# Kernel tuning notes

Hardware: AMD Instinct MI355X
Metric: run time of the kernel (lower is better)

Reference implementation:

```python
import jax, jax.numpy as jnp
import numpy as np

N_NODES = 50000
N_EDGES = 800000
QRY = 128
KEY = 128
VAL = 128
HEADS = 8
HEAD_FEATS = VAL // HEADS
BN_EPS = 1e-5


def setup_inputs() -> dict:
    key = jax.random.key(0)
    ks = jax.random.split(key, 12)
    inp = {
        "ft_q": jax.random.normal(ks[0], (N_NODES, QRY), dtype=jnp.float32),
        "ft_k": jax.random.normal(ks[1], (N_NODES, KEY), dtype=jnp.float32),
        "src": jax.random.randint(ks[2], (N_EDGES,), 0, N_NODES, dtype=jnp.int32),
        "dst": jax.random.randint(ks[3], (N_EDGES,), 0, N_NODES, dtype=jnp.int32),
        # learned params
        "Wq": jax.random.normal(ks[4], (VAL, QRY), dtype=jnp.float32) / np.sqrt(QRY),
        "bq": jnp.zeros((VAL,), dtype=jnp.float32),
        "Wk": jax.random.normal(ks[5], (VAL, KEY), dtype=jnp.float32) / np.sqrt(KEY),
        "Wv": jax.random.normal(ks[6], (VAL, QRY), dtype=jnp.float32) / np.sqrt(QRY),
        "attn_e": jax.random.normal(ks[7], (VAL,), dtype=jnp.float32),
        "bn_q_g": jnp.ones((QRY,), dtype=jnp.float32),
        "bn_q_b": jnp.zeros((QRY,), dtype=jnp.float32),
        "bn_k_g": jnp.ones((KEY,), dtype=jnp.float32),
        "bn_k_b": jnp.zeros((KEY,), dtype=jnp.float32),
    }
    return inp


def _batch_norm(x, gamma, beta):
    # training-mode BatchNorm1d: normalize over batch dim
    mean = jnp.mean(x, axis=0, keepdims=True)
    var = jnp.var(x, axis=0, keepdims=True)
    return (x - mean) * jax.lax.rsqrt(var + BN_EPS) * gamma + beta


def reference(ft_q, ft_k, src, dst, Wq, bq, Wk, Wv, attn_e,
              bn_q_g, bn_q_b, bn_k_g, bn_k_b):
    ft_q = _batch_norm(ft_q, bn_q_g, bn_q_b)
    ft_k = _batch_norm(ft_k, bn_k_g, bn_k_b)

    q = ft_q @ Wq.T + bq                      # [N, VAL]
    k = ft_k @ Wk.T                           # [N, VAL]
    v = (ft_q @ Wv.T).reshape(-1, HEADS, HEAD_FEATS)  # [N, H, D]

    # u_add_v: per-edge e = q[src] + k[dst]
    e = q[src] + k[dst]                       # [E, VAL]
    e = (attn_e * jax.nn.sigmoid(e)).reshape(-1, HEADS, HEAD_FEATS).sum(-1)  # [E, H]

    # edge_softmax grouped by destination node
    m = jax.ops.segment_max(e, dst, num_segments=N_NODES)   # [N, H]
    ex = jnp.exp(e - m[dst])                                # [E, H]
    s = jax.ops.segment_sum(ex, dst, num_segments=N_NODES)  # [N, H]
    a = ex / s[dst]                                         # [E, H]

    # u_mul_e_sum: scatter-sum of v[src] * a over destination
    msg = v[src] * a[:, :, None]                            # [E, H, D]
    rst = jax.ops.segment_sum(msg, dst, num_segments=N_NODES)  # [N, H, D]
    return rst.reshape(-1, VAL)
```

## Files before the change

### kernel.cpp

```cpp
#include <hip/hip_runtime.h>

#define N_NODES 50000
#define N_EDGES 800000
#define FEATS 128
#define NCHUNK 196
#define CPAD 50176
#define GEMM_BX 196
#define GEMM_BLOCKS 588
#define SCAT_BLOCKS 3125
#define NTILE 782
#define NF_WAVES 8192

typedef __attribute__((ext_vector_type(8))) short bf16x8;
typedef __attribute__((ext_vector_type(4))) float f32x4;

__device__ __forceinline__ unsigned short f2bf(float f){
  unsigned u = __float_as_uint(f);
  u += 0x7FFF + ((u >> 16) & 1);
  return (unsigned short)(u >> 16);
}
__device__ __forceinline__ void unpack8(uint4 p, float* f){
  f[0]=__uint_as_float(p.x << 16); f[1]=__uint_as_float(p.x & 0xffff0000u);
  f[2]=__uint_as_float(p.y << 16); f[3]=__uint_as_float(p.y & 0xffff0000u);
  f[4]=__uint_as_float(p.z << 16); f[5]=__uint_as_float(p.z & 0xffff0000u);
  f[6]=__uint_as_float(p.w << 16); f[7]=__uint_as_float(p.w & 0xffff0000u);
}

__global__ __launch_bounds__(256) void stats_hist_kernel(
    const float* __restrict__ ftq, const float* __restrict__ ftk,
    float* __restrict__ sums, const int* __restrict__ dstE,
    int* __restrict__ counts, int* __restrict__ csums){
  __shared__ float red[4*FEATS];
  __shared__ int lchunk[NCHUNK];
  int tid = threadIdx.x, bid = blockIdx.x;
  if (bid < 768){
    for (int i = tid; i < 4*FEATS; i += 256) red[i] = 0.f;
    __syncthreads();
    int c = tid & 127, half = tid >> 7;
    float sq=0.f, qq=0.f, sk=0.f, kk2=0.f;
    for (int r = bid*2 + half; r < N_NODES; r += 1536){
      float xq = ftq[(size_t)r*FEATS + c];
      float xk = ftk[(size_t)r*FEATS + c];
      sq += xq; qq += xq*xq; sk += xk; kk2 += xk*xk;
    }
    atomicAdd(&red[0*FEATS+c], sq);
    atomicAdd(&red[1*FEATS+c], qq);
    atomicAdd(&red[2*FEATS+c], sk);
    atomicAdd(&red[3*FEATS+c], kk2);
    __syncthreads();
    if (tid < FEATS){
      atomicAdd(&sums[0*FEATS+tid], red[0*FEATS+tid]);
      atomicAdd(&sums[1*FEATS+tid], red[1*FEATS+tid]);
      atomicAdd(&sums[2*FEATS+tid], red[2*FEATS+tid]);
      atomicAdd(&sums[3*FEATS+tid], red[3*FEATS+tid]);
    }
  } else {
    for (int i = tid; i < NCHUNK; i += 256) lchunk[i] = 0;
    __syncthreads();
    for (int t = (bid-768)*256 + tid; t < N_EDGES; t += 256*256){
      int d = dstE[t];
      atomicAdd(&counts[d], 1);
      atomicAdd(&lchunk[d >> 8], 1);
    }
    __syncthreads();
    for (int i = tid; i < NCHUNK; i += 256)
      if (lchunk[i]) atomicAdd(&csums[i], lchunk[i]);
  }
}

__global__ __launch_bounds__(256) void scan_fold_kernel(
    const int* __restrict__ counts, const int* __restrict__ csums,
    int* __restrict__ loc, int* __restrict__ bscan,
    const float* __restrict__ Wq, const float* __restrict__ bq,
    const float* __restrict__ Wk, const float* __restrict__ Wv,
    const float* __restrict__ gq, const float* __restrict__ bqn,
    const float* __restrict__ gk, const float* __restrict__ bkn,
    const float* __restrict__ sums,
    unsigned short* __restrict__ Wb, float* __restrict__ bias){
  __shared__ int s[256];
  int tid = threadIdx.x, bid = blockIdx.x;
  if (bid < NCHUNK){
    int i = bid*256 + tid;
    int v = counts[i];
    s[tid] = v; __syncthreads();
    for (int d = 1; d < 256; d <<= 1){
      int tv = (tid >= d) ? s[tid-d] : 0; __syncthreads();
      s[tid] += tv; __syncthreads();
    }
    loc[i] = s[tid] - v;
  } else if (bid == NCHUNK){
    int v = (tid < NCHUNK) ? csums[tid] : 0;
    s[tid] = v; __syncthreads();
    for (int d = 1; d < 256; d <<= 1){
      int tv = (tid >= d) ? s[tid-d] : 0; __syncthreads();
      s[tid] += tv; __syncthreads();
    }
    if (tid < NCHUNK) bscan[tid] = s[tid] - v;
  } else {
    int wv = (bid - NCHUNK - 1)*4 + (tid >> 6);
    int lane = tid & 63;
    int m = wv >> 7;
    int o = wv & 127;
    const float* Wsrc = (m==0) ? Wq : (m==1) ? Wv : Wk;
    const float* g   = (m==2) ? gk : gq;
    const float* bb  = (m==2) ? bkn : bqn;
    const float* s0  = (m==2) ? (sums + 2*FEATS) : sums;
    const float invN = 1.0f / (float)N_NODES;
    float acc = 0.f;
    unsigned short w2[2];
    int i0 = lane*2;
    #pragma unroll
    for (int t = 0; t < 2; t++){
      int i = i0 + t;
      float mean = s0[i]*invN;
      float var  = s0[FEATS+i]*invN - mean*mean;
      float rstd = rsqrtf(var + 1e-5f);
      float scale = g[i]*rstd;
      float shift = bb[i] - mean*scale;
      float w = Wsrc[o*FEATS + i];
      w2[t] = f2bf(w*scale);
      acc += shift*w;
    }
    ((unsigned*)Wb)[(m*FEATS*FEATS + o*FEATS + i0) >> 1] =
        (unsigned)w2[0] | ((unsigned)w2[1] << 16);
    #pragma unroll
    for (int off = 1; off < 64; off <<= 1) acc += __shfl_xor(acc, off);
    if (lane == 0) bias[m*FEATS + o] = acc + ((m==0) ? bq[o] : 0.f);
  }
}

__global__ __launch_bounds__(256) void gemm_scatter_kernel(
    const float* __restrict__ ftq, const float* __restrict__ ftk,
    const unsigned short* __restrict__ Wball, const float* __restrict__ biasall,
    unsigned short* __restrict__ qv, unsigned short* __restrict__ kb,
    const int* __restrict__ dstE, const int* __restrict__ srcE,
    const int* __restrict__ loc, const int* __restrict__ bscan,
    int* __restrict__ cursor, int* __restrict__ src_csr){
  __shared__ unsigned short Bs[FEATS][136];
  int tid = threadIdx.x, bid = blockIdx.x;
  if (bid >= GEMM_BLOCKS){
    int t = (bid - GEMM_BLOCKS)*256 + tid;
    int d = dstE[t];
    int p = atomicAdd(&cursor[d], 1);
    src_csr[loc[d] + bscan[d >> 8] + p] = srcE[t];
    return;
  }
  int m = bid / GEMM_BX;
  int bx = bid - m*GEMM_BX;
  const float* X = (m==2) ? ftk : ftq;
  {
    const uint4* srcp = (const uint4*)(Wball + m*FEATS*FEATS);
    for (int idx = tid; idx < FEATS*FEATS/8; idx += 256){
      int n = idx >> 4;
      int kk = (idx & 15) * 8;
      *(uint4*)&Bs[n][kk] = srcp[idx];
    }
  }
  __syncthreads();
  int wave = tid >> 6, lane = tid & 63;
  int mrow = lane & 15, quad = lane >> 4;
  unsigned short* Out = (m==2) ? kb : (qv + m*128);
  const int ostride = (m==2) ? FEATS : 256;
  float bv[8];
  #pragma unroll
  for (int ct = 0; ct < 8; ct++) bv[ct] = biasall[m*FEATS + ct*16 + mrow];
  for (int t = bx; t < NTILE; t += GEMM_BX){
    int row0 = t*64;
    int arow = row0 + wave*16 + mrow;
    bool rok = arow < N_NODES;
    size_t abase = (size_t)(rok ? arow : 0) * FEATS;
    bf16x8 afrag[4];
    #pragma unroll
    for (int kt = 0; kt < 4; kt++){
      const float* xp = X + abase + kt*32 + quad*8;
      float4 x0 = *(const float4*)xp;
      float4 x1 = *(const float4*)(xp + 4);
      if (!rok){ x0 = make_float4(0.f,0.f,0.f,0.f); x1 = x0; }
      bf16x8 a;
      a[0]=(short)f2bf(x0.x); a[1]=(short)f2bf(x0.y); a[2]=(short)f2bf(x0.z); a[3]=(short)f2bf(x0.w);
      a[4]=(short)f2bf(x1.x); a[5]=(short)f2bf(x1.y); a[6]=(short)f2bf(x1.z); a[7]=(short)f2bf(x1.w);
      afrag[kt] = a;
    }
    f32x4 acc[8];
    #pragma unroll
    for (int i = 0; i < 8; i++) acc[i] = (f32x4){0.f,0.f,0.f,0.f};
    #pragma unroll
    for (int kt = 0; kt < 4; kt++){
      int kbk = kt*32 + quad*8;
      #pragma unroll
      for (int ct = 0; ct < 8; ct++){
        bf16x8 b = *(bf16x8*)&Bs[ct*16 + mrow][kbk];
        acc[ct] = __builtin_amdgcn_mfma_f32_16x16x32_bf16(afrag[kt], b, acc[ct], 0, 0, 0);
      }
    }
    #pragma unroll
    for (int ct = 0; ct < 8; ct++){
      int col = ct*16 + mrow;
      #pragma unroll
      for (int v = 0; v < 4; v++){
        int orow = row0 + wave*16 + quad*4 + v;
        unsigned ub = f2bf(acc[ct][v] + bv[ct]);
        unsigned partner = (unsigned)__shfl_xor((int)ub, 1);
        if (!(mrow & 1) && orow < N_NODES)
          *(unsigned*)&Out[(size_t)orow*ostride + col] = ub | (partner << 16);
      }
    }
  }
}

__global__ __launch_bounds__(256) void node_fused_kernel(
    const unsigned short* __restrict__ qv, const unsigned short* __restrict__ kb,
    const float* __restrict__ attn, const int* __restrict__ src_csr,
    const int* __restrict__ loc, const int* __restrict__ bscan,
    float* __restrict__ out){
  int tid = threadIdx.x;
  int lane = tid & 63;
  int h = lane & 7, g = lane >> 3;
  int w = blockIdx.x*4 + (tid >> 6);
  const float L2E = 1.44269504f;
  float ar[16];
  {
    const uint4* ap = (const uint4*)(attn + h*16);
    uint4 a0 = ap[0], a1 = ap[1], a2 = ap[2], a3 = ap[3];
    ar[0]=__uint_as_float(a0.x); ar[1]=__uint_as_float(a0.y); ar[2]=__uint_as_float(a0.z); ar[3]=__uint_as_float(a0.w);
    ar[4]=__uint_as_float(a1.x); ar[5]=__uint_as_float(a1.y); ar[6]=__uint_as_float(a1.z); ar[7]=__uint_as_float(a1.w);
    ar[8]=__uint_as_float(a2.x); ar[9]=__uint_as_float(a2.y); ar[10]=__uint_as_float(a2.z); ar[11]=__uint_as_float(a2.w);
    ar[12]=__uint_as_float(a3.x); ar[13]=__uint_as_float(a3.y); ar[14]=__uint_as_float(a3.z); ar[15]=__uint_as_float(a3.w);
  }
  for (int n = w; n < N_NODES; n += NF_WAVES){
    int off0 = loc[n]   + bscan[n>>8];
    int off1 = loc[n+1] + bscan[(n+1)>>8];
    int deg = off1 - off0;
    if (deg == 0){
      ((float2*)(out + (size_t)n*FEATS))[lane] = make_float2(0.f, 0.f);
      continue;
    }
    float kf2[16];
    {
      const unsigned short* kr = kb + (size_t)n*FEATS + h*16;
      uint4 k0 = *(const uint4*)kr;
      uint4 k1 = *(const uint4*)(kr + 8);
      float kf[16]; unpack8(k0, kf); unpack8(k1, kf+8);
      #pragma unroll
      for (int i = 0; i < 16; i++) kf2[i] = -L2E * kf[i];
    }
    float ssum = 0.f;
    float acc[16];
    #pragma unroll
    for (int i = 0; i < 16; i++) acc[i] = 0.f;
    int s_next = (g < deg) ? src_csr[off0 + g] : 0;
    for (int j = g; j < deg; j += 8){
      int s = s_next;
      if (j + 8 < deg) s_next = src_csr[off0 + j + 8];
      const unsigned short* qr = qv + (size_t)s*256 + h*16;
      uint4 q0 = *(const uint4*)qr;
      uint4 q1 = *(const uint4*)(qr + 8);
      uint4 v0 = *(const uint4*)(qr + 128);
      uint4 v1 = *(const uint4*)(qr + 136);
      float qf[16]; unpack8(q0, qf); unpack8(q1, qf+8);
      float t = 0.f;
      #pragma unroll
      for (int i = 0; i < 16; i++){
        float xs = fmaf(qf[i], -L2E, kf2[i]);
        float sg = __builtin_amdgcn_rcpf(1.f + __builtin_amdgcn_exp2f(xs));
        t = fmaf(ar[i], sg, t);
      }
      float ex = __builtin_amdgcn_exp2f(t * L2E);
      ssum += ex;
      float vf[16]; unpack8(v0, vf); unpack8(v1, vf+8);
      #pragma unroll
      for (int i = 0; i < 16; i++) acc[i] = fmaf(ex, vf[i], acc[i]);
    }
    ssum += __shfl_xor(ssum, 8); ssum += __shfl_xor(ssum, 16); ssum += __shfl_xor(ssum, 32);
    #pragma unroll
    for (int i = 0; i < 16; i++){
      acc[i] += __shfl_xor(acc[i], 8);
      acc[i] += __shfl_xor(acc[i], 16);
      acc[i] += __shfl_xor(acc[i], 32);
    }
    if (g == 0){
      float inv_s = 1.f / ssum;
      float4* op = (float4*)(out + (size_t)n*FEATS + h*16);
      op[0] = make_float4(acc[0]*inv_s, acc[1]*inv_s, acc[2]*inv_s, acc[3]*inv_s);
      op[1] = make_float4(acc[4]*inv_s, acc[5]*inv_s, acc[6]*inv_s, acc[7]*inv_s);
      op[2] = make_float4(acc[8]*inv_s, acc[9]*inv_s, acc[10]*inv_s, acc[11]*inv_s);
      op[3] = make_float4(acc[12]*inv_s, acc[13]*inv_s, acc[14]*inv_s, acc[15]*inv_s);
    }
  }
}

extern "C" void kernel_launch(void* const* d_in, const int* in_sizes, int n_in,
                              void* d_out, int out_size, void* d_ws, size_t ws_size,
                              hipStream_t stream){
  (void)in_sizes; (void)n_in; (void)out_size; (void)ws_size;
  const float* ftq  = (const float*)d_in[0];
  const float* ftk  = (const float*)d_in[1];
  const int*   srcE = (const int*)d_in[2];
  const int*   dstE = (const int*)d_in[3];
  const float* Wq   = (const float*)d_in[4];
  const float* bq   = (const float*)d_in[5];
  const float* Wk   = (const float*)d_in[6];
  const float* Wv   = (const float*)d_in[7];
  const float* attn = (const float*)d_in[8];
  const float* gq   = (const float*)d_in[9];
  const float* bqn  = (const float*)d_in[10];
  const float* gk   = (const float*)d_in[11];
  const float* bkn  = (const float*)d_in[12];

  char* ws = (char*)d_ws;
  int*   counts  = (int*)(ws + 0);
  int*   cursor  = (int*)(ws + 200704);
  float* sums    = (float*)(ws + 400704);
  int*   csums   = (int*)(ws + 402752);
  int*   loc     = (int*)(ws + 403536);
  int*   bscan   = (int*)(ws + 604240);
  int*   src_csr = (int*)(ws + 605024);
  unsigned short* Wb = (unsigned short*)(ws + 3805024);
  float* biasf   = (float*)(ws + 3903328);
  unsigned short* qv = (unsigned short*)(ws + 3904864);
  unsigned short* kb = qv + (size_t)N_NODES*256;
  float* out = (float*)d_out;

  hipMemsetAsync(ws, 0, 403536, stream);

  hipLaunchKernelGGL(stats_hist_kernel, dim3(1024), dim3(256), 0, stream,
                     ftq, ftk, sums, dstE, counts, csums);
  hipLaunchKernelGGL(scan_fold_kernel, dim3(293), dim3(256), 0, stream,
                     counts, csums, loc, bscan,
                     Wq, bq, Wk, Wv, gq, bqn, gk, bkn, sums, Wb, biasf);
  hipLaunchKernelGGL(gemm_scatter_kernel, dim3(GEMM_BLOCKS + SCAT_BLOCKS), dim3(256), 0, stream,
                     ftq, ftk, Wb, biasf, qv, kb, dstE, srcE, loc, bscan, cursor, src_csr);
  hipLaunchKernelGGL(node_fused_kernel, dim3(NF_WAVES/4), dim3(256), 0, stream,
                     qv, kb, attn, src_csr, loc, bscan, out);
}
```

Baseline: 290.2 us.

## Record edge ranks in histogram, vectorize BN stats, prefetch GEMM tiles and gathers

```diff
diff --git a/kernel.cpp b/kernel.cpp
--- a/kernel.cpp
+++ b/kernel.cpp
@@ -10,6 +10,8 @@
 #define SCAT_BLOCKS 3125
 #define NTILE 782
 #define NF_WAVES 8192
+#define STAT_BLOCKS 256
+#define HIST_BLOCKS 512
 
 typedef __attribute__((ext_vector_type(8))) short bf16x8;
 typedef __attribute__((ext_vector_type(4))) float f32x4;
@@ -29,37 +31,44 @@
 __global__ __launch_bounds__(256) void stats_hist_kernel(
     const float* __restrict__ ftq, const float* __restrict__ ftk,
     float* __restrict__ sums, const int* __restrict__ dstE,
-    int* __restrict__ counts, int* __restrict__ csums){
+    int* __restrict__ counts, int* __restrict__ csums,
+    unsigned short* __restrict__ rankE){
   __shared__ float red[4*FEATS];
   __shared__ int lchunk[NCHUNK];
   int tid = threadIdx.x, bid = blockIdx.x;
-  if (bid < 768){
+  if (bid < STAT_BLOCKS){
     for (int i = tid; i < 4*FEATS; i += 256) red[i] = 0.f;
     __syncthreads();
-    int c = tid & 127, half = tid >> 7;
-    float sq=0.f, qq=0.f, sk=0.f, kk2=0.f;
-    for (int r = bid*2 + half; r < N_NODES; r += 1536){
-      float xq = ftq[(size_t)r*FEATS + c];
-      float xk = ftk[(size_t)r*FEATS + c];
-      sq += xq; qq += xq*xq; sk += xk; kk2 += xk*xk;
-    }
-    atomicAdd(&red[0*FEATS+c], sq);
-    atomicAdd(&red[1*FEATS+c], qq);
-    atomicAdd(&red[2*FEATS+c], sk);
-    atomicAdd(&red[3*FEATS+c], kk2);
+    int sub = tid >> 5, c4 = tid & 31;
+    const float* Xs = (sub < 4) ? ftq : ftk;
+    int so = (sub < 4) ? 0 : 2*FEATS;
+    float a0=0,a1=0,a2=0,a3=0,b0=0,b1=0,b2=0,b3=0;
+    #pragma unroll 4
+    for (int r = bid*4 + (sub&3); r < N_NODES; r += STAT_BLOCKS*4){
+      float4 x = *(const float4*)(Xs + (size_t)r*FEATS + c4*4);
+      a0+=x.x; b0+=x.x*x.x; a1+=x.y; b1+=x.y*x.y;
+      a2+=x.z; b2+=x.z*x.z; a3+=x.w; b3+=x.w*x.w;
+    }
+    a0 += __shfl_xor(a0,32); a1 += __shfl_xor(a1,32);
+    a2 += __shfl_xor(a2,32); a3 += __shfl_xor(a3,32);
+    b0 += __shfl_xor(b0,32); b1 += __shfl_xor(b1,32);
+    b2 += __shfl_xor(b2,32); b3 += __shfl_xor(b3,32);
+    if ((tid & 63) < 32){
+      int c0 = c4*4;
+      atomicAdd(&red[so + c0+0], a0); atomicAdd(&red[so + c0+1], a1);
+      atomicAdd(&red[so + c0+2], a2); atomicAdd(&red[so + c0+3], a3);
+      atomicAdd(&red[so + FEATS + c0+0], b0); atomicAdd(&red[so + FEATS + c0+1], b1);
+      atomicAdd(&red[so + FEATS + c0+2], b2); atomicAdd(&red[so + FEATS + c0+3], b3);
+    }
     __syncthreads();
-    if (tid < FEATS){
-      atomicAdd(&sums[0*FEATS+tid], red[0*FEATS+tid]);
-      atomicAdd(&sums[1*FEATS+tid], red[1*FEATS+tid]);
-      atomicAdd(&sums[2*FEATS+tid], red[2*FEATS+tid]);
-      atomicAdd(&sums[3*FEATS+tid], red[3*FEATS+tid]);
-    }
+    for (int i = tid; i < 4*FEATS; i += 256) atomicAdd(&sums[i], red[i]);
   } else {
     for (int i = tid; i < NCHUNK; i += 256) lchunk[i] = 0;
     __syncthreads();
-    for (int t = (bid-768)*256 + tid; t < N_EDGES; t += 256*256){
+    for (int t = (bid-STAT_BLOCKS)*256 + tid; t < N_EDGES; t += HIST_BLOCKS*256){
       int d = dstE[t];
-      atomicAdd(&counts[d], 1);
+      int p = atomicAdd(&counts[d], 1);
+      rankE[t] = (unsigned short)p;
       atomicAdd(&lchunk[d >> 8], 1);
     }
     __syncthreads();
@@ -135,14 +144,13 @@
     unsigned short* __restrict__ qv, unsigned short* __restrict__ kb,
     const int* __restrict__ dstE, const int* __restrict__ srcE,
     const int* __restrict__ loc, const int* __restrict__ bscan,
-    int* __restrict__ cursor, int* __restrict__ src_csr){
+    const unsigned short* __restrict__ rankE, int* __restrict__ src_csr){
   __shared__ unsigned short Bs[FEATS][136];
   int tid = threadIdx.x, bid = blockIdx.x;
   if (bid >= GEMM_BLOCKS){
     int t = (bid - GEMM_BLOCKS)*256 + tid;
     int d = dstE[t];
-    int p = atomicAdd(&cursor[d], 1);
-    src_csr[loc[d] + bscan[d >> 8] + p] = srcE[t];
+    src_csr[loc[d] + bscan[d >> 8] + (int)rankE[t]] = srcE[t];
     return;
   }
   int m = bid / GEMM_BX;
@@ -164,35 +172,40 @@
   float bv[8];
   #pragma unroll
   for (int ct = 0; ct < 8; ct++) bv[ct] = biasall[m*FEATS + ct*16 + mrow];
+  float4 cur[8], nxt[8];
+  auto loadx = [&](float4* buf, int t){
+    int arow = t*64 + wave*16 + mrow;
+    bool rok = arow < N_NODES;
+    const float* xp = X + (size_t)(rok ? arow : 0)*FEATS + quad*8;
+    #pragma unroll
+    for (int kt = 0; kt < 4; kt++){
+      float4 x0 = *(const float4*)(xp + kt*32);
+      float4 x1 = *(const float4*)(xp + kt*32 + 4);
+      if (!rok){ x0 = make_float4(0.f,0.f,0.f,0.f); x1 = x0; }
+      buf[2*kt] = x0; buf[2*kt+1] = x1;
+    }
+  };
+  loadx(cur, bx);
   for (int t = bx; t < NTILE; t += GEMM_BX){
-    int row0 = t*64;
-    int arow = row0 + wave*16 + mrow;
-    bool rok = arow < N_NODES;
-    size_t abase = (size_t)(rok ? arow : 0) * FEATS;
-    bf16x8 afrag[4];
+    int tn = t + GEMM_BX;
+    if (tn < NTILE) loadx(nxt, tn);
+    f32x4 acc[8];
+    #pragma unroll
+    for (int i = 0; i < 8; i++) acc[i] = (f32x4){0.f,0.f,0.f,0.f};
     #pragma unroll
     for (int kt = 0; kt < 4; kt++){
-      const float* xp = X + abase + kt*32 + quad*8;
-      float4 x0 = *(const float4*)xp;
-      float4 x1 = *(const float4*)(xp + 4);
-      if (!rok){ x0 = make_float4(0.f,0.f,0.f,0.f); x1 = x0; }
+      float4 x0 = cur[2*kt], x1 = cur[2*kt+1];
       bf16x8 a;
       a[0]=(short)f2bf(x0.x); a[1]=(short)f2bf(x0.y); a[2]=(short)f2bf(x0.z); a[3]=(short)f2bf(x0.w);
       a[4]=(short)f2bf(x1.x); a[5]=(short)f2bf(x1.y); a[6]=(short)f2bf(x1.z); a[7]=(short)f2bf(x1.w);
-      afrag[kt] = a;
-    }
-    f32x4 acc[8];
-    #pragma unroll
-    for (int i = 0; i < 8; i++) acc[i] = (f32x4){0.f,0.f,0.f,0.f};
-    #pragma unroll
-    for (int kt = 0; kt < 4; kt++){
       int kbk = kt*32 + quad*8;
       #pragma unroll
       for (int ct = 0; ct < 8; ct++){
         bf16x8 b = *(bf16x8*)&Bs[ct*16 + mrow][kbk];
-        acc[ct] = __builtin_amdgcn_mfma_f32_16x16x32_bf16(afrag[kt], b, acc[ct], 0, 0, 0);
+        acc[ct] = __builtin_amdgcn_mfma_f32_16x16x32_bf16(a, b, acc[ct], 0, 0, 0);
       }
     }
+    int row0 = t*64;
     #pragma unroll
     for (int ct = 0; ct < 8; ct++){
       int col = ct*16 + mrow;
@@ -205,6 +218,8 @@
           *(unsigned*)&Out[(size_t)orow*ostride + col] = ub | (partner << 16);
       }
     }
+    #pragma unroll
+    for (int i = 0; i < 8; i++) cur[i] = nxt[i];
   }
 }
 
@@ -248,28 +263,38 @@
     float acc[16];
     #pragma unroll
     for (int i = 0; i < 16; i++) acc[i] = 0.f;
-    int s_next = (g < deg) ? src_csr[off0 + g] : 0;
-    for (int j = g; j < deg; j += 8){
-      int s = s_next;
-      if (j + 8 < deg) s_next = src_csr[off0 + j + 8];
-      const unsigned short* qr = qv + (size_t)s*256 + h*16;
-      uint4 q0 = *(const uint4*)qr;
-      uint4 q1 = *(const uint4*)(qr + 8);
-      uint4 v0 = *(const uint4*)(qr + 128);
-      uint4 v1 = *(const uint4*)(qr + 136);
-      float qf[16]; unpack8(q0, qf); unpack8(q1, qf+8);
-      float t = 0.f;
-      #pragma unroll
-      for (int i = 0; i < 16; i++){
-        float xs = fmaf(qf[i], -L2E, kf2[i]);
-        float sg = __builtin_amdgcn_rcpf(1.f + __builtin_amdgcn_exp2f(xs));
-        t = fmaf(ar[i], sg, t);
+    if (g < deg){
+      int sA = src_csr[off0 + g];
+      int jB = g + 8;
+      int sB = (jB < deg) ? src_csr[off0 + jB] : sA;
+      const unsigned short* pA = qv + (size_t)sA*256 + h*16;
+      uint4 qa0 = *(const uint4*)pA;
+      uint4 qa1 = *(const uint4*)(pA + 8);
+      while (true){
+        uint4 va0 = *(const uint4*)(pA + 128);
+        uint4 va1 = *(const uint4*)(pA + 136);
+        const unsigned short* pB = qv + (size_t)sB*256 + h*16;
+        uint4 qb0 = *(const uint4*)pB;
+        uint4 qb1 = *(const uint4*)(pB + 8);
+        int jC = jB + 8;
+        int sC = (jC < deg) ? src_csr[off0 + jC] : sB;
+        float qf[16]; unpack8(qa0, qf); unpack8(qa1, qf+8);
+        float t = 0.f;
+        #pragma unroll
+        for (int i = 0; i < 16; i++){
+          float xs = fmaf(qf[i], -L2E, kf2[i]);
+          float sg = __builtin_amdgcn_rcpf(1.f + __builtin_amdgcn_exp2f(xs));
+          t = fmaf(ar[i], sg, t);
+        }
+        float ex = __builtin_amdgcn_exp2f(t * L2E);
+        ssum += ex;
+        float vf[16]; unpack8(va0, vf); unpack8(va1, vf+8);
+        #pragma unroll
+        for (int i = 0; i < 16; i++) acc[i] = fmaf(ex, vf[i], acc[i]);
+        if (jB >= deg) break;
+        qa0 = qb0; qa1 = qb1; pA = pB;
+        jB = jC; sB = sC;
       }
-      float ex = __builtin_amdgcn_exp2f(t * L2E);
-      ssum += ex;
-      float vf[16]; unpack8(v0, vf); unpack8(v1, vf+8);
-      #pragma unroll
-      for (int i = 0; i < 16; i++) acc[i] = fmaf(ex, vf[i], acc[i]);
     }
     ssum += __shfl_xor(ssum, 8); ssum += __shfl_xor(ssum, 16); ssum += __shfl_xor(ssum, 32);
     #pragma unroll
@@ -309,27 +334,27 @@
 
   char* ws = (char*)d_ws;
   int*   counts  = (int*)(ws + 0);
-  int*   cursor  = (int*)(ws + 200704);
-  float* sums    = (float*)(ws + 400704);
-  int*   csums   = (int*)(ws + 402752);
-  int*   loc     = (int*)(ws + 403536);
-  int*   bscan   = (int*)(ws + 604240);
-  int*   src_csr = (int*)(ws + 605024);
-  unsigned short* Wb = (unsigned short*)(ws + 3805024);
-  float* biasf   = (float*)(ws + 3903328);
-  unsigned short* qv = (unsigned short*)(ws + 3904864);
+  float* sums    = (float*)(ws + 200704);
+  int*   csums   = (int*)(ws + 202752);
+  int*   loc     = (int*)(ws + 203536);
+  int*   bscan   = (int*)(ws + 404240);
+  int*   src_csr = (int*)(ws + 405024);
+  unsigned short* rankE = (unsigned short*)(ws + 3605024);
+  unsigned short* Wb = (unsigned short*)(ws + 5205024);
+  float* biasf   = (float*)(ws + 5303328);
+  unsigned short* qv = (unsigned short*)(ws + 5304864);
   unsigned short* kb = qv + (size_t)N_NODES*256;
   float* out = (float*)d_out;
 
-  hipMemsetAsync(ws, 0, 403536, stream);
-
-  hipLaunchKernelGGL(stats_hist_kernel, dim3(1024), dim3(256), 0, stream,
-                     ftq, ftk, sums, dstE, counts, csums);
+  hipMemsetAsync(ws, 0, 203536, stream);
+
+  hipLaunchKernelGGL(stats_hist_kernel, dim3(STAT_BLOCKS + HIST_BLOCKS), dim3(256), 0, stream,
+                     ftq, ftk, sums, dstE, counts, csums, rankE);
   hipLaunchKernelGGL(scan_fold_kernel, dim3(293), dim3(256), 0, stream,
                      counts, csums, loc, bscan,
                      Wq, bq, Wk, Wv, gq, bqn, gk, bkn, sums, Wb, biasf);
   hipLaunchKernelGGL(gemm_scatter_kernel, dim3(GEMM_BLOCKS + SCAT_BLOCKS), dim3(256), 0, stream,
-                     ftq, ftk, Wb, biasf, qv, kb, dstE, srcE, loc, bscan, cursor, src_csr);
+                     ftq, ftk, Wb, biasf, qv, kb, dstE, srcE, loc, bscan, rankE, src_csr);
   hipLaunchKernelGGL(node_fused_kernel, dim3(NF_WAVES/4), dim3(256), 0, stream,
                      qv, kb, attn, src_csr, loc, bscan, out);
 }
```

Measured after the change: 277.0 us. 1.05x faster.
